# Kernel optimization log

Hardware: AMD Instinct MI355X
Metric: run time of the kernel (lower is better)

Reference implementation:

```python
import jax, jax.numpy as jnp
import numpy as np

V, E, H, OUT = 100000, 300, 256, 3
B, LS, LT = 128, 128, 8


def _lstm_scan(xs, Wih, Whh, bih, bhh, reverse):
    # xs: [T, B, E] time-major; returns hidden states [T, B, H] in original time order
    h0 = jnp.zeros((xs.shape[1], H), xs.dtype)
    def step(carry, x):
        h, c = carry
        g = x @ Wih.T + bih + h @ Whh.T + bhh  # [B, 4H]
        i, f, gg, o = jnp.split(g, 4, axis=-1)
        c = jax.nn.sigmoid(f) * c + jax.nn.sigmoid(i) * jnp.tanh(gg)
        h = jax.nn.sigmoid(o) * jnp.tanh(c)
        return (h, c), h
    _, hs = jax.lax.scan(step, (h0, h0), xs, reverse=reverse)
    return hs


def _bidir(emb_bte, Wih_f, Whh_f, bih_f, bhh_f, Wih_b, Whh_b, bih_b, bhh_b):
    xs = jnp.transpose(emb_bte, (1, 0, 2))  # [T, B, E]
    hf = _lstm_scan(xs, Wih_f, Whh_f, bih_f, bhh_f, False)
    hb = _lstm_scan(xs, Wih_b, Whh_b, bih_b, bhh_b, True)
    return jnp.transpose(jnp.concatenate([hf, hb], axis=-1), (1, 0, 2))  # [B, T, 2H]


def setup_inputs() -> dict:
    key = jax.random.key(0)
    ks = jax.random.split(key, 32)
    n = lambda i, shape: 0.05 * jax.random.normal(ks[i], shape, dtype=jnp.float32)
    inp = {
        "sentence_source": jax.random.randint(ks[0], (B, LS), 0, V),
        "target_source": jax.random.randint(ks[1], (B, LT), 0, V),
        "emb_W": n(2, (V, E)),
    }
    names = ["sf", "sb", "tf", "tb"]
    for j, nm in enumerate(names):
        base = 3 + 4 * j
        inp[f"Wih_{nm}"] = n(base + 0, (4 * H, E))
        inp[f"Whh_{nm}"] = n(base + 1, (4 * H, H))
        inp[f"bih_{nm}"] = n(base + 2, (4 * H,))
        inp[f"bhh_{nm}"] = n(base + 3, (4 * H,))
    inp["Wout"] = n(20, (OUT, 2 * H))
    inp["bout"] = n(21, (OUT,))
    return inp


def reference(sentence_source, target_source, emb_W,
              Wih_sf, Whh_sf, bih_sf, bhh_sf,
              Wih_sb, Whh_sb, bih_sb, bhh_sb,
              Wih_tf, Whh_tf, bih_tf, bhh_tf,
              Wih_tb, Whh_tb, bih_tb, bhh_tb,
              Wout, bout):
    emb = emb_W.at[0].set(0.0)  # padding_idx=0
    sen = emb[sentence_source]  # [B, LS, E]  (dropout is identity at eval)
    tgt = emb[target_source]    # [B, LT, E]
    sen_h = _bidir(sen, Wih_sf, Whh_sf, bih_sf, bhh_sf, Wih_sb, Whh_sb, bih_sb, bhh_sb)  # [B, LS, 2H]
    tgt_h = _bidir(tgt, Wih_tf, Whh_tf, bih_tf, bhh_tf, Wih_tb, Whh_tb, bih_tb, bhh_tb)  # [B, LT, 2H]
    A = jnp.einsum("bsh,bth->bst", sen_h, tgt_h)          # [B, LS, LT]
    col = jax.nn.softmax(A, axis=1)
    row = jax.nn.softmax(A, axis=2)
    row_vec = jnp.mean(row, axis=1, keepdims=True)         # [B, 1, LT]
    attn = jnp.einsum("bst,bqt->bsq", col, row_vec)        # [B, LS, 1]
    score = jnp.einsum("bsq,bsh->bqh", attn, sen_h)        # [B, 1, 2H]
    logits = score @ Wout.T + bout                         # [B, 1, OUT]
    return jax.nn.softmax(logits, axis=-1).squeeze()       # [B, OUT]
```

## Files before the change

### kernel.cpp

```cpp
#include <hip/hip_runtime.h>


typedef unsigned short u16;
typedef unsigned long long u64;
typedef float f32x4 __attribute__((ext_vector_type(4)));
typedef int   i32x4 __attribute__((ext_vector_type(4)));
typedef short bf16x8 __attribute__((ext_vector_type(8)));
typedef short s16x4 __attribute__((ext_vector_type(4)));
typedef unsigned short u16x4 __attribute__((ext_vector_type(4)));

#define KP 320
#define KPL 328
#define FH 1024
#define HH 256
#define L2E 1.4426950408889634f

struct Ptr4 { const float* p[4]; };

static __device__ __forceinline__ u16 f2bf(float f) {
    unsigned int u = __float_as_uint(f);
    u += 0x7FFFu + ((u >> 16) & 1u);
    return (u16)(u >> 16);
}
static __device__ __forceinline__ float bf2f(u16 s) {
    return __uint_as_float((unsigned int)s << 16);
}
static __device__ __forceinline__ float sigm2(float x) {
    return __builtin_amdgcn_rcpf(1.0f + __builtin_amdgcn_exp2f(-x));
}
static __device__ __forceinline__ float tanh2(float x) {
    return 1.0f - 2.0f * __builtin_amdgcn_rcpf(1.0f + __builtin_amdgcn_exp2f(x));
}

__global__ __launch_bounds__(256) void pre_kernel(
    const int* __restrict__ sen, const int* __restrict__ tgt,
    const float* __restrict__ emb, Ptr4 Wih, Ptr4 Whh, Ptr4 bih, Ptr4 bhh,
    u16* __restrict__ Xs, u16* __restrict__ Xt,
    u16* __restrict__ WihB, float* __restrict__ biasB,
    char* __restrict__ Wq, float* __restrict__ wdq)
{
    int bid = blockIdx.x, tid = threadIdx.x;
    if (bid < 17408) {
        int row = bid;
        int tok; u16* dst;
        if (row < 16384) { tok = sen[row]; dst = Xs + (size_t)row * KP; }
        else             { tok = tgt[row - 16384]; dst = Xt + (size_t)(row - 16384) * KP; }
        const float* src = emb + (size_t)tok * 300;
        for (int k = tid; k < KP; k += 256) {
            float v = (k < 300 && tok != 0) ? src[k] : 0.0f;
            dst[k] = f2bf(v);
        }
    } else if (bid < 22528) {
        int local = bid - 17408;
        int dir = local / 1280, blk = local - dir * 1280;
        int idx = blk * 256 + tid;
        if (idx < FH * KP) {
            int row = idx / KP, k = idx - row * KP;
            float gsc = ((row >> 8) == 2) ? 2.0f * L2E : L2E;
            WihB[(size_t)dir * FH * KP + idx] =
                (k < 300) ? f2bf(Wih.p[dir][row * 300 + k] * gsc) : (u16)0;
        }
        if (idx < FH) {
            float gsc = ((idx >> 8) == 2) ? 2.0f * L2E : L2E;
            biasB[dir * FH + idx] = (bih.p[dir][idx] + bhh.p[dir][idx]) * gsc;
        }
    } else {
        int local = bid - 22528;
        int w = tid >> 6, lane = tid & 63;
        int pair = local * 4 + w;
        int dir = pair >> 10, row = pair & 1023;
        const float* src = Whh.p[dir] + (size_t)row * HH;
        float m = 0.0f;
        for (int k = lane; k < HH; k += 64) m = fmaxf(m, fabsf(src[k]));
        for (int off = 32; off; off >>= 1) m = fmaxf(m, __shfl_down(m, off));
        m = __shfl(m, 0);
        float qs = (m > 0.0f) ? 127.0f / m : 0.0f;
        char* dst = Wq + (size_t)dir * FH * HH + (size_t)row * HH;
        for (int k = lane; k < HH; k += 64) dst[k] = (char)(int)rintf(src[k] * qs);
        if (lane == 0) {
            float gsc = ((row >> 8) == 2) ? 2.0f * L2E : L2E;
            wdq[dir * FH + row] = (m > 0.0f) ? m / (127.0f * 127.0f) * gsc : 0.0f;
        }
    }
}

__global__ __launch_bounds__(256) void input_gemm_kernel(
    const u16* __restrict__ Xs, const u16* __restrict__ Xt,
    const u16* __restrict__ WihB, const float* __restrict__ biasB,
    u16* __restrict__ Gs, u16* __restrict__ Gt)
{
    __shared__ u16 Bs[64][KPL];

    int bid = blockIdx.x;
    const u16* X; const u16* W; const float* bias; u16* G;
    int lbid, nwg, tsh;
    if (bid < 4096) { lbid = bid;        nwg = 4096; tsh = 7;
                      X = Xs; W = WihB;                         bias = biasB;          G = Gs; }
    else            { lbid = bid - 4096; nwg = 256;  tsh = 3;
                      X = Xt; W = WihB + (size_t)2 * FH * KP;   bias = biasB + 2 * FH; G = Gt; }

    int cpx = nwg >> 3;
    int wid = (lbid & 7) * cpx + (lbid >> 3);
    int nblk = wid & 31;
    int mblk = wid >> 5;
    int dirb = nblk >> 4;
    int u0   = (nblk & 15) * 16;
    size_t dirStride = (size_t)(tsh == 7 ? 16384 : 1024) * FH;

    int tid = threadIdx.x;
    int wave = tid >> 6, lane = tid & 63;
    int r = lane & 15, quad = lane >> 4;
    int m0 = mblk * 128 + wave * 32;

#pragma unroll
    for (int it = 0; it < 10; ++it) {
        int idx = it * 256 + tid;
        int row = idx / 40, cc = idx - row * 40;
        int j = row >> 4, rr = row & 15;
        bf16x8 v = *(const bf16x8*)(W + ((size_t)dirb * FH + j * 256 + u0 + rr) * KP + cc * 8);
        *(bf16x8*)&Bs[row][cc * 8] = v;
    }
    __syncthreads();

    const u16* xr = X + (size_t)(m0 + r) * KP + quad * 8;
    f32x4 acc[2][4] = {};
#pragma unroll
    for (int k0 = 0; k0 < KP; k0 += 32) {
        bf16x8 a0 = *(const bf16x8*)(xr + k0);
        bf16x8 a1 = *(const bf16x8*)(xr + 16 * KP + k0);
#pragma unroll
        for (int j = 0; j < 4; ++j) {
            bf16x8 b = *(const bf16x8*)&Bs[j * 16 + r][k0 + quad * 8];
            acc[0][j] = __builtin_amdgcn_mfma_f32_16x16x32_bf16(a0, b, acc[0][j], 0, 0, 0);
            acc[1][j] = __builtin_amdgcn_mfma_f32_16x16x32_bf16(a1, b, acc[1][j], 0, 0, 0);
        }
    }

#pragma unroll
    for (int sub = 0; sub < 2; ++sub)
#pragma unroll
        for (int reg = 0; reg < 4; ++reg) {
            int m = m0 + sub * 16 + quad * 4 + reg;
            int b = m >> tsh, t = m & ((1 << tsh) - 1);
            int unit = u0 + r;
            u16x4 ov;
#pragma unroll
            for (int j = 0; j < 4; ++j)
                ov[j] = f2bf(acc[sub][j][reg] + bias[dirb * FH + j * 256 + unit]);
            *(u16x4*)(G + (size_t)dirb * dirStride + ((size_t)t * 128 + b) * FH + unit * 4) = ov;
        }
}

__global__ __launch_bounds__(1024, 1) void lstm_scan_kernel(
    const char*  __restrict__ WqB,
    const float* __restrict__ wdq,
    const u16*   __restrict__ Gs,
    const u16*   __restrict__ Gt,
    float* __restrict__ senH,
    float* __restrict__ tgtH)
{
    const int bx  = blockIdx.x;
    const int dir = bx >> 3;
    const int b0  = (bx & 7) << 4;
    const int T   = (dir < 2) ? 128 : 8;
    const int rev = dir & 1;

    const char* Wq = WqB + (size_t)dir * FH * HH;
    const u16*  G  = (dir < 2) ? (Gs + (size_t)dir * 16384 * FH)
                               : (Gt + (size_t)(dir - 2) * 1024 * FH);
    float* Hout = (dir < 2) ? senH : tgtH;
    const int hofs = rev ? 256 : 0;

    const int tid  = threadIdx.x;
    const int w    = tid >> 6, lane = tid & 63;
    const int r    = lane & 15, quad = lane >> 4;
    const int u    = w * 16 + r;

    __shared__ __align__(16) char hb8[2][16][272];

    i32x4 Bq[4][4];
    float dqv[4];
#pragma unroll
    for (int g = 0; g < 4; ++g) {
        int row = g * 256 + u;
        dqv[g] = wdq[dir * FH + row];
#pragma unroll
        for (int kt = 0; kt < 4; ++kt)
            Bq[g][kt] = *(const i32x4*)(Wq + ((size_t)row << 8) + kt * 64 + quad * 16);
    }

    for (int i = tid; i < 2 * 16 * 272; i += 1024) (&hb8[0][0][0])[i] = 0;
    __syncthreads();

    float c[4] = {};
    float hreg[4] = {};

    const int t0 = rev ? (T - 1) : 0;
    const ptrdiff_t gstep = rev ? -(ptrdiff_t)(128 * FH) : (ptrdiff_t)(128 * FH);
    const ptrdiff_t hstep = rev ? -(ptrdiff_t)(128 * 512) : (ptrdiff_t)(128 * 512);
    const u16* gp0 = G + ((size_t)t0 * 128 + b0 + quad * 4) * FH + u * 4;
    const u16* gp2 = gp0 + 2 * (size_t)FH;
    float* hp0 = Hout + ((size_t)t0 * 128 + b0 + quad * 4) * 512 + hofs + u;
    float* hp2 = hp0 + 2 * 512;

    s16x4 gvA[4], gvB[4];
    gvA[0] = *(const s16x4*)(gp0);
    gvA[1] = *(const s16x4*)(gp0 + FH);
    gvA[2] = *(const s16x4*)(gp2);
    gvA[3] = *(const s16x4*)(gp2 + FH);
    gp0 += gstep; gp2 += gstep;

    auto body = [&](int cur, s16x4 (&gvU)[4], s16x4 (&gvP)[4], int doStore) {
        gvP[0] = *(const s16x4*)(gp0);
        gvP[1] = *(const s16x4*)(gp0 + FH);
        gvP[2] = *(const s16x4*)(gp2);
        gvP[3] = *(const s16x4*)(gp2 + FH);
        gp0 += gstep; gp2 += gstep;
        if (doStore) {
            hp0[0] = hreg[0]; hp0[512] = hreg[1];
            hp2[0] = hreg[2]; hp2[512] = hreg[3];
            hp0 += hstep; hp2 += hstep;
        }

        i32x4 acc[4] = {};
#pragma unroll
        for (int kt = 0; kt < 4; ++kt) {
            i32x4 a = *(const i32x4*)&hb8[cur][r][kt * 64 + quad * 16];
#pragma unroll
            for (int g = 0; g < 4; ++g)
                acc[g] = __builtin_amdgcn_mfma_i32_16x16x64_i8(a, Bq[g][kt], acc[g], 0, 0, 0);
        }

#pragma unroll
        for (int reg = 0; reg < 4; ++reg) {
            int bb = quad * 4 + reg;
            float pi = (float)acc[0][reg] * dqv[0] + bf2f((u16)gvU[reg].x);
            float pf = (float)acc[1][reg] * dqv[1] + bf2f((u16)gvU[reg].y);
            float pg = (float)acc[2][reg] * dqv[2] + bf2f((u16)gvU[reg].z);
            float po = (float)acc[3][reg] * dqv[3] + bf2f((u16)gvU[reg].w);
            float ig = sigm2(pi), fg = sigm2(pf), gg = tanh2(pg), og = sigm2(po);
            float cn = fg * c[reg] + ig * gg;
            c[reg] = cn;
            float hn = og * tanh2(cn * (2.0f * L2E));
            hb8[cur ^ 1][bb][u] = (char)(int)rintf(hn * 127.0f);
            hreg[reg] = hn;
        }
        __syncthreads();
    };

    for (int s2 = 0; s2 < T; s2 += 2) {
        body(0, gvA, gvB, s2 > 0);
        body(1, gvB, gvA, 1);
    }

    hp0[0] = hreg[0]; hp0[512] = hreg[1];
    hp2[0] = hreg[2]; hp2[512] = hreg[3];
}

__global__ __launch_bounds__(256) void attn_out_kernel(
    const float* __restrict__ senH, const float* __restrict__ tgtH,
    const float* __restrict__ Wout, const float* __restrict__ bout,
    float* __restrict__ out)
{
    int b = blockIdx.x, tid = threadIdx.x;
    __shared__ float tg[8][512];
    __shared__ float Am[128][9];
    __shared__ float rowm[128][9];
    __shared__ float mcol[8], csum[8], rvec[8], attn[128], score[512], lg[3];

    for (int i = tid; i < 4096; i += 256) {
        int t = i >> 9, h = i & 511;
        tg[t][h] = tgtH[((size_t)t * 128 + b) * 512 + h];
    }
    __syncthreads();

    {
        int s = tid >> 1, t0 = (tid & 1) * 4;
        const float* sr = senH + ((size_t)s * 128 + b) * 512;
        float d0 = 0, d1 = 0, d2 = 0, d3 = 0;
        for (int h = 0; h < 512; ++h) {
            float x = sr[h];
            d0 += x * tg[t0 + 0][h]; d1 += x * tg[t0 + 1][h];
            d2 += x * tg[t0 + 2][h]; d3 += x * tg[t0 + 3][h];
        }
        Am[s][t0 + 0] = d0; Am[s][t0 + 1] = d1; Am[s][t0 + 2] = d2; Am[s][t0 + 3] = d3;
    }
    __syncthreads();

    if (tid < 8) {
        float m = -1e30f;
        for (int s = 0; s < 128; ++s) m = fmaxf(m, Am[s][tid]);
        float sum = 0;
        for (int s = 0; s < 128; ++s) sum += __expf(Am[s][tid] - m);
        mcol[tid] = m; csum[tid] = sum;
    }
    if (tid >= 64 && tid < 192) {
        int s = tid - 64;
        float m = -1e30f;
        for (int t = 0; t < 8; ++t) m = fmaxf(m, Am[s][t]);
        float e[8], sum = 0;
        for (int t = 0; t < 8; ++t) { e[t] = __expf(Am[s][t] - m); sum += e[t]; }
        float inv = __builtin_amdgcn_rcpf(sum);
        for (int t = 0; t < 8; ++t) rowm[s][t] = e[t] * inv;
    }
    __syncthreads();
    if (tid < 8) {
        float sum = 0;
        for (int s = 0; s < 128; ++s) sum += rowm[s][tid];
        rvec[tid] = sum * (1.0f / 128.0f);
    }
    __syncthreads();
    if (tid < 128) {
        float a = 0;
        for (int t = 0; t < 8; ++t)
            a += __expf(Am[tid][t] - mcol[t]) / csum[t] * rvec[t];
        attn[tid] = a;
    }
    __syncthreads();
    for (int h = tid; h < 512; h += 256) {
        float acc = 0;
        const float* sp = senH + b * 512 + h;
        for (int s = 0; s < 128; ++s) acc += attn[s] * sp[(size_t)s * 128 * 512];
        score[h] = acc;
    }
    __syncthreads();
    if (tid < 3) {
        float acc = bout[tid];
        const float* wr = Wout + tid * 512;
        for (int h = 0; h < 512; ++h) acc += score[h] * wr[h];
        lg[tid] = acc;
    }
    __syncthreads();
    if (tid == 0) {
        float m = fmaxf(lg[0], fmaxf(lg[1], lg[2]));
        float e0 = __expf(lg[0] - m), e1 = __expf(lg[1] - m), e2 = __expf(lg[2] - m);
        float inv = 1.0f / (e0 + e1 + e2);
        out[b * 3 + 0] = e0 * inv; out[b * 3 + 1] = e1 * inv; out[b * 3 + 2] = e2 * inv;
    }
}

extern "C" void kernel_launch(void* const* d_in, const int* in_sizes, int n_in,
                              void* d_out, int out_size, void* d_ws, size_t ws_size,
                              hipStream_t stream)
{
    const int*   sen = (const int*)d_in[0];
    const int*   tgt = (const int*)d_in[1];
    const float* emb = (const float*)d_in[2];
    Ptr4 Wih = {{(const float*)d_in[3],  (const float*)d_in[7],
                 (const float*)d_in[11], (const float*)d_in[15]}};
    Ptr4 Whh = {{(const float*)d_in[4],  (const float*)d_in[8],
                 (const float*)d_in[12], (const float*)d_in[16]}};
    Ptr4 bih = {{(const float*)d_in[5],  (const float*)d_in[9],
                 (const float*)d_in[13], (const float*)d_in[17]}};
    Ptr4 bhh = {{(const float*)d_in[6],  (const float*)d_in[10],
                 (const float*)d_in[14], (const float*)d_in[18]}};
    const float* Wout = (const float*)d_in[19];
    const float* bout = (const float*)d_in[20];
    float* out = (float*)d_out;

    char* ws = (char*)d_ws;
    size_t off = 0;
    auto alloc = [&](size_t bytes) -> void* {
        void* p = ws + off; off += (bytes + 255) & ~(size_t)255; return p;
    };
    u16*   Xs    = (u16*)alloc((size_t)16384 * KP * 2);
    u16*   Xt    = (u16*)alloc((size_t)1024 * KP * 2);
    u16*   WihB  = (u16*)alloc((size_t)4 * FH * KP * 2);
    char*  WqB   = (char*)alloc((size_t)4 * FH * HH);
    float* wdq   = (float*)alloc((size_t)4 * FH * 4);
    float* biasB = (float*)alloc((size_t)4 * FH * 4);
    u16*   Gs    = (u16*)alloc((size_t)2 * 16384 * FH * 2);
    u16*   Gt    = (u16*)alloc((size_t)2 * 1024 * FH * 2);
    float* senH  = (float*)alloc((size_t)128 * 128 * 512 * 4);
    float* tgtH  = (float*)alloc((size_t)128 * 8 * 512 * 4);
    (void)ws_size; (void)in_sizes; (void)n_in; (void)out_size;

    pre_kernel<<<23552, 256, 0, stream>>>(sen, tgt, emb, Wih, Whh, bih, bhh,
                                          Xs, Xt, WihB, biasB, WqB, wdq);
    input_gemm_kernel<<<4352, 256, 0, stream>>>(Xs, Xt, WihB, biasB, Gs, Gt);
    lstm_scan_kernel<<<32, 1024, 0, stream>>>(WqB, wdq, Gs, Gt, senH, tgtH);
    attn_out_kernel<<<128, 256, 0, stream>>>(senH, tgtH, Wout, bout, out);
}
```

Baseline: 503.9 us.

## Split sentence LSTM hidden units across workgroup pairs with global-memory flag sync

```diff
diff --git a/kernel.cpp b/kernel.cpp
--- a/kernel.cpp
+++ b/kernel.cpp
@@ -2,6 +2,7 @@
 
 
 typedef unsigned short u16;
+typedef unsigned int u32;
 typedef unsigned long long u64;
 typedef float f32x4 __attribute__((ext_vector_type(4)));
 typedef int   i32x4 __attribute__((ext_vector_type(4)));
@@ -37,7 +38,8 @@
     const float* __restrict__ emb, Ptr4 Wih, Ptr4 Whh, Ptr4 bih, Ptr4 bhh,
     u16* __restrict__ Xs, u16* __restrict__ Xt,
     u16* __restrict__ WihB, float* __restrict__ biasB,
-    char* __restrict__ Wq, float* __restrict__ wdq)
+    char* __restrict__ Wq, float* __restrict__ wdq,
+    char* __restrict__ hx, u32* __restrict__ prog)
 {
     int bid = blockIdx.x, tid = threadIdx.x;
     if (bid < 17408) {
@@ -64,7 +66,7 @@
             float gsc = ((idx >> 8) == 2) ? 2.0f * L2E : L2E;
             biasB[dir * FH + idx] = (bih.p[dir][idx] + bhh.p[dir][idx]) * gsc;
         }
-    } else {
+    } else if (bid < 23552) {
         int local = bid - 22528;
         int w = tid >> 6, lane = tid & 63;
         int pair = local * 4 + w;
@@ -81,6 +83,12 @@
             float gsc = ((row >> 8) == 2) ? 2.0f * L2E : L2E;
             wdq[dir * FH + row] = (m > 0.0f) ? m / (127.0f * 127.0f) * gsc : 0.0f;
         }
+    } else if (bid < 23584) {
+        int local = bid - 23552;
+        f32x4 z = {};
+        *(f32x4*)(hx + (size_t)local * 4096 + tid * 16) = z;
+    } else {
+        if (tid < 32) prog[tid] = 0;
     }
 }
 
@@ -151,110 +159,213 @@
         }
 }
 
-__global__ __launch_bounds__(1024, 1) void lstm_scan_kernel(
+__global__ __launch_bounds__(512, 2) void lstm_scan_kernel(
     const char*  __restrict__ WqB,
     const float* __restrict__ wdq,
     const u16*   __restrict__ Gs,
     const u16*   __restrict__ Gt,
     float* __restrict__ senH,
-    float* __restrict__ tgtH)
+    float* __restrict__ tgtH,
+    char*  __restrict__ hx,
+    u32*   __restrict__ prog)
 {
     const int bx  = blockIdx.x;
-    const int dir = bx >> 3;
-    const int b0  = (bx & 7) << 4;
-    const int T   = (dir < 2) ? 128 : 8;
-    const int rev = dir & 1;
-
-    const char* Wq = WqB + (size_t)dir * FH * HH;
-    const u16*  G  = (dir < 2) ? (Gs + (size_t)dir * 16384 * FH)
-                               : (Gt + (size_t)(dir - 2) * 1024 * FH);
-    float* Hout = (dir < 2) ? senH : tgtH;
-    const int hofs = rev ? 256 : 0;
-
-    const int tid  = threadIdx.x;
+    const int tid = threadIdx.x;
     const int w    = tid >> 6, lane = tid & 63;
     const int r    = lane & 15, quad = lane >> 4;
-    const int u    = w * 16 + r;
-
-    __shared__ __align__(16) char hb8[2][16][272];
-
-    i32x4 Bq[4][4];
-    float dqv[4];
-#pragma unroll
-    for (int g = 0; g < 4; ++g) {
-        int row = g * 256 + u;
-        dqv[g] = wdq[dir * FH + row];
-#pragma unroll
-        for (int kt = 0; kt < 4; ++kt)
-            Bq[g][kt] = *(const i32x4*)(Wq + ((size_t)row << 8) + kt * 64 + quad * 16);
-    }
-
-    for (int i = tid; i < 2 * 16 * 272; i += 1024) (&hb8[0][0][0])[i] = 0;
-    __syncthreads();
-
-    float c[4] = {};
-    float hreg[4] = {};
-
-    const int t0 = rev ? (T - 1) : 0;
-    const ptrdiff_t gstep = rev ? -(ptrdiff_t)(128 * FH) : (ptrdiff_t)(128 * FH);
-    const ptrdiff_t hstep = rev ? -(ptrdiff_t)(128 * 512) : (ptrdiff_t)(128 * 512);
-    const u16* gp0 = G + ((size_t)t0 * 128 + b0 + quad * 4) * FH + u * 4;
-    const u16* gp2 = gp0 + 2 * (size_t)FH;
-    float* hp0 = Hout + ((size_t)t0 * 128 + b0 + quad * 4) * 512 + hofs + u;
-    float* hp2 = hp0 + 2 * 512;
-
-    s16x4 gvA[4], gvB[4];
-    gvA[0] = *(const s16x4*)(gp0);
-    gvA[1] = *(const s16x4*)(gp0 + FH);
-    gvA[2] = *(const s16x4*)(gp2);
-    gvA[3] = *(const s16x4*)(gp2 + FH);
-    gp0 += gstep; gp2 += gstep;
-
-    auto body = [&](int cur, s16x4 (&gvU)[4], s16x4 (&gvP)[4], int doStore) {
-        gvP[0] = *(const s16x4*)(gp0);
-        gvP[1] = *(const s16x4*)(gp0 + FH);
-        gvP[2] = *(const s16x4*)(gp2);
-        gvP[3] = *(const s16x4*)(gp2 + FH);
+
+    __shared__ __align__(16) char hb[2][16][272];
+
+    for (int i = tid; i < 2 * 16 * 272; i += 512) (&hb[0][0][0])[i] = 0;
+    __syncthreads();
+
+    if (bx < 32) {
+        const int dir   = bx >> 4;
+        const int chunk = (bx >> 1) & 7;
+        const int ph    = bx & 1;
+        const int b0    = chunk << 4;
+        const int rev   = dir & 1;
+        const int T     = 128;
+
+        const char* Wq = WqB + (size_t)dir * FH * HH;
+        const u16*  G  = Gs + (size_t)dir * 16384 * FH;
+        const int hofs = rev ? 256 : 0;
+        const int uloc = w * 16 + r;
+        const int ug   = ph * 128 + uloc;
+
+        const int pairI = dir * 8 + chunk;
+        char* sliceW = hx + ((size_t)(pairI * 2 + ph) * 2) * 2048;
+        char* sliceR = hx + ((size_t)(pairI * 2 + (1 - ph)) * 2) * 2048;
+        u32* progMe = prog + pairI * 2 + ph;
+        u32* progP  = prog + pairI * 2 + (1 - ph);
+
+        i32x4 Bq[4][4];
+        float dqv[4];
+#pragma unroll
+        for (int g = 0; g < 4; ++g) {
+            int row = g * 256 + ug;
+            dqv[g] = wdq[dir * FH + row];
+#pragma unroll
+            for (int j = 0; j < 4; ++j) {
+                int kt = (j < 2) ? (ph * 2 + j) : ((1 - ph) * 2 + (j - 2));
+                Bq[g][j] = *(const i32x4*)(Wq + ((size_t)row << 8) + kt * 64 + quad * 16);
+            }
+        }
+
+        float c[4] = {}, hreg[4] = {};
+
+        const int t0 = rev ? (T - 1) : 0;
+        const ptrdiff_t gstep = rev ? -(ptrdiff_t)(128 * FH) : (ptrdiff_t)(128 * FH);
+        const ptrdiff_t hstep = rev ? -(ptrdiff_t)(128 * 512) : (ptrdiff_t)(128 * 512);
+        const u16* gp0 = G + ((size_t)t0 * 128 + b0 + quad * 4) * FH + ug * 4;
+        const u16* gp2 = gp0 + 2 * (size_t)FH;
+        float* hp0 = senH + ((size_t)t0 * 128 + b0 + quad * 4) * 512 + hofs + ug;
+        float* hp2 = hp0 + 2 * 512;
+
+        s16x4 gvA[4], gvB[4];
+        gvA[0] = *(const s16x4*)(gp0);
+        gvA[1] = *(const s16x4*)(gp0 + FH);
+        gvA[2] = *(const s16x4*)(gp2);
+        gvA[3] = *(const s16x4*)(gp2 + FH);
         gp0 += gstep; gp2 += gstep;
-        if (doStore) {
-            hp0[0] = hreg[0]; hp0[512] = hreg[1];
-            hp2[0] = hreg[2]; hp2[512] = hreg[3];
-            hp0 += hstep; hp2 += hstep;
-        }
-
-        i32x4 acc[4] = {};
-#pragma unroll
-        for (int kt = 0; kt < 4; ++kt) {
-            i32x4 a = *(const i32x4*)&hb8[cur][r][kt * 64 + quad * 16];
-#pragma unroll
-            for (int g = 0; g < 4; ++g)
-                acc[g] = __builtin_amdgcn_mfma_i32_16x16x64_i8(a, Bq[g][kt], acc[g], 0, 0, 0);
-        }
-
-#pragma unroll
-        for (int reg = 0; reg < 4; ++reg) {
-            int bb = quad * 4 + reg;
-            float pi = (float)acc[0][reg] * dqv[0] + bf2f((u16)gvU[reg].x);
-            float pf = (float)acc[1][reg] * dqv[1] + bf2f((u16)gvU[reg].y);
-            float pg = (float)acc[2][reg] * dqv[2] + bf2f((u16)gvU[reg].z);
-            float po = (float)acc[3][reg] * dqv[3] + bf2f((u16)gvU[reg].w);
-            float ig = sigm2(pi), fg = sigm2(pf), gg = tanh2(pg), og = sigm2(po);
-            float cn = fg * c[reg] + ig * gg;
-            c[reg] = cn;
-            float hn = og * tanh2(cn * (2.0f * L2E));
-            hb8[cur ^ 1][bb][u] = (char)(int)rintf(hn * 127.0f);
-            hreg[reg] = hn;
-        }
-        __syncthreads();
-    };
-
-    for (int s2 = 0; s2 < T; s2 += 2) {
-        body(0, gvA, gvB, s2 > 0);
-        body(1, gvB, gvA, 1);
-    }
-
-    hp0[0] = hreg[0]; hp0[512] = hreg[1];
-    hp2[0] = hreg[2]; hp2[512] = hreg[3];
+
+        auto body = [&](int cur, s16x4 (&gvU)[4], s16x4 (&gvP)[4], int s, int doStore) {
+            gvP[0] = *(const s16x4*)(gp0);
+            gvP[1] = *(const s16x4*)(gp0 + FH);
+            gvP[2] = *(const s16x4*)(gp2);
+            gvP[3] = *(const s16x4*)(gp2 + FH);
+            gp0 += gstep; gp2 += gstep;
+            if (doStore) {
+                hp0[0] = hreg[0]; hp0[512] = hreg[1];
+                hp2[0] = hreg[2]; hp2[512] = hreg[3];
+                hp0 += hstep; hp2 += hstep;
+            }
+
+            i32x4 aO0 = *(const i32x4*)&hb[cur][r][quad * 16];
+            i32x4 aO1 = *(const i32x4*)&hb[cur][r][64 + quad * 16];
+
+            if (s > 0)
+                while (__hip_atomic_load(progP, __ATOMIC_ACQUIRE,
+                                         __HIP_MEMORY_SCOPE_AGENT) < (u32)s)
+                    __builtin_amdgcn_s_sleep(1);
+            char* sr = sliceR + (cur ^ 1) * 2048 + r * 128 + quad * 16;
+            u64 p00 = __hip_atomic_load((u64*)(sr),      __ATOMIC_RELAXED, __HIP_MEMORY_SCOPE_AGENT);
+            u64 p01 = __hip_atomic_load((u64*)(sr + 8),  __ATOMIC_RELAXED, __HIP_MEMORY_SCOPE_AGENT);
+            u64 p10 = __hip_atomic_load((u64*)(sr + 64), __ATOMIC_RELAXED, __HIP_MEMORY_SCOPE_AGENT);
+            u64 p11 = __hip_atomic_load((u64*)(sr + 72), __ATOMIC_RELAXED, __HIP_MEMORY_SCOPE_AGENT);
+            i32x4 aP0, aP1;
+            ((u64*)&aP0)[0] = p00; ((u64*)&aP0)[1] = p01;
+            ((u64*)&aP1)[0] = p10; ((u64*)&aP1)[1] = p11;
+
+            i32x4 acc[4] = {};
+#pragma unroll
+            for (int g = 0; g < 4; ++g) {
+                acc[g] = __builtin_amdgcn_mfma_i32_16x16x64_i8(aO0, Bq[g][0], acc[g], 0, 0, 0);
+                acc[g] = __builtin_amdgcn_mfma_i32_16x16x64_i8(aO1, Bq[g][1], acc[g], 0, 0, 0);
+                acc[g] = __builtin_amdgcn_mfma_i32_16x16x64_i8(aP0, Bq[g][2], acc[g], 0, 0, 0);
+                acc[g] = __builtin_amdgcn_mfma_i32_16x16x64_i8(aP1, Bq[g][3], acc[g], 0, 0, 0);
+            }
+
+            char* sw = sliceW + cur * 2048 + uloc;
+#pragma unroll
+            for (int reg = 0; reg < 4; ++reg) {
+                int bb = quad * 4 + reg;
+                float pi = (float)acc[0][reg] * dqv[0] + bf2f((u16)gvU[reg].x);
+                float pf = (float)acc[1][reg] * dqv[1] + bf2f((u16)gvU[reg].y);
+                float pg = (float)acc[2][reg] * dqv[2] + bf2f((u16)gvU[reg].z);
+                float po = (float)acc[3][reg] * dqv[3] + bf2f((u16)gvU[reg].w);
+                float ig = sigm2(pi), fg = sigm2(pf), gg = tanh2(pg), og = sigm2(po);
+                float cn = fg * c[reg] + ig * gg;
+                c[reg] = cn;
+                float hn = og * tanh2(cn * (2.0f * L2E));
+                char q = (char)(int)rintf(hn * 127.0f);
+                hb[cur ^ 1][bb][uloc] = q;
+                __hip_atomic_store(sw + bb * 128, q, __ATOMIC_RELAXED,
+                                   __HIP_MEMORY_SCOPE_AGENT);
+                hreg[reg] = hn;
+            }
+            __syncthreads();
+            if (tid == 0)
+                __hip_atomic_store(progMe, (u32)(s + 1), __ATOMIC_RELEASE,
+                                   __HIP_MEMORY_SCOPE_AGENT);
+        };
+
+        for (int s2 = 0; s2 < T; s2 += 2) {
+            body(0, gvA, gvB, s2, s2 > 0);
+            body(1, gvB, gvA, s2 + 1, 1);
+        }
+        hp0[0] = hreg[0]; hp0[512] = hreg[1];
+        hp2[0] = hreg[2]; hp2[512] = hreg[3];
+    } else {
+        const int lb    = bx - 32;
+        const int dir   = 2 + (lb >> 3);
+        const int chunk = lb & 7;
+        const int b0    = chunk << 4;
+        const int rev   = dir & 1;
+
+        const char* Wq = WqB + (size_t)dir * FH * HH;
+        const u16*  G  = Gt + (size_t)(dir - 2) * 1024 * FH;
+        const int hofs = rev ? 256 : 0;
+
+        i32x4 Bq2[2][4][4];
+        float dqv2[2][4];
+#pragma unroll
+        for (int su = 0; su < 2; ++su)
+#pragma unroll
+            for (int g = 0; g < 4; ++g) {
+                int row = g * 256 + w * 32 + su * 16 + r;
+                dqv2[su][g] = wdq[dir * FH + row];
+#pragma unroll
+                for (int kt = 0; kt < 4; ++kt)
+                    Bq2[su][g][kt] = *(const i32x4*)(Wq + ((size_t)row << 8) + kt * 64 + quad * 16);
+            }
+
+        float c2[2][4] = {};
+        for (int s = 0; s < 8; ++s) {
+            const int t = rev ? (7 - s) : s;
+            const int cur = s & 1;
+            s16x4 gv[2][4];
+#pragma unroll
+            for (int su = 0; su < 2; ++su)
+#pragma unroll
+                for (int reg = 0; reg < 4; ++reg)
+                    gv[su][reg] = *(const s16x4*)(G + ((size_t)t * 128 + b0 + quad * 4 + reg) * FH
+                                                  + (w * 32 + su * 16 + r) * 4);
+            i32x4 af[4];
+#pragma unroll
+            for (int kt = 0; kt < 4; ++kt)
+                af[kt] = *(const i32x4*)&hb[cur][r][kt * 64 + quad * 16];
+
+            i32x4 acc[2][4] = {};
+#pragma unroll
+            for (int su = 0; su < 2; ++su)
+#pragma unroll
+                for (int g = 0; g < 4; ++g)
+#pragma unroll
+                    for (int kt = 0; kt < 4; ++kt)
+                        acc[su][g] = __builtin_amdgcn_mfma_i32_16x16x64_i8(
+                            af[kt], Bq2[su][g][kt], acc[su][g], 0, 0, 0);
+
+#pragma unroll
+            for (int su = 0; su < 2; ++su)
+#pragma unroll
+                for (int reg = 0; reg < 4; ++reg) {
+                    int bb = quad * 4 + reg;
+                    int u = w * 32 + su * 16 + r;
+                    float pi = (float)acc[su][0][reg] * dqv2[su][0] + bf2f((u16)gv[su][reg].x);
+                    float pf = (float)acc[su][1][reg] * dqv2[su][1] + bf2f((u16)gv[su][reg].y);
+                    float pg = (float)acc[su][2][reg] * dqv2[su][2] + bf2f((u16)gv[su][reg].z);
+                    float po = (float)acc[su][3][reg] * dqv2[su][3] + bf2f((u16)gv[su][reg].w);
+                    float ig = sigm2(pi), fg = sigm2(pf), gg = tanh2(pg), og = sigm2(po);
+                    float cn = fg * c2[su][reg] + ig * gg;
+                    c2[su][reg] = cn;
+                    float hn = og * tanh2(cn * (2.0f * L2E));
+                    hb[cur ^ 1][bb][u] = (char)(int)rintf(hn * 127.0f);
+                    tgtH[((size_t)t * 128 + b0 + bb) * 512 + hofs + u] = hn;
+                }
+            __syncthreads();
+        }
+    }
 }
 
 __global__ __launch_bounds__(256) void attn_out_kernel(
@@ -373,11 +484,13 @@
     u16*   Gt    = (u16*)alloc((size_t)2 * 1024 * FH * 2);
     float* senH  = (float*)alloc((size_t)128 * 128 * 512 * 4);
     float* tgtH  = (float*)alloc((size_t)128 * 8 * 512 * 4);
+    char*  hx    = (char*)alloc((size_t)131072);
+    u32*   prog  = (u32*)alloc((size_t)128);
     (void)ws_size; (void)in_sizes; (void)n_in; (void)out_size;
 
-    pre_kernel<<<23552, 256, 0, stream>>>(sen, tgt, emb, Wih, Whh, bih, bhh,
-                                          Xs, Xt, WihB, biasB, WqB, wdq);
+    pre_kernel<<<23585, 256, 0, stream>>>(sen, tgt, emb, Wih, Whh, bih, bhh,
+                                          Xs, Xt, WihB, biasB, WqB, wdq, hx, prog);
     input_gemm_kernel<<<4352, 256, 0, stream>>>(Xs, Xt, WihB, biasB, Gs, Gt);
-    lstm_scan_kernel<<<32, 1024, 0, stream>>>(WqB, wdq, Gs, Gt, senH, tgtH);
+    lstm_scan_kernel<<<48, 512, 0, stream>>>(WqB, wdq, Gs, Gt, senH, tgtH, hx, prog);
     attn_out_kernel<<<128, 256, 0, stream>>>(senH, tgtH, Wout, bout, out);
 }
```

After: 1.078 ms. 2.14x slower.
